# Kernel optimization log

Hardware: AMD Instinct MI355X
Metric: run time of the kernel (lower is better)

The kernel has to match this reference:

```python
import jax, jax.numpy as jnp
import numpy as np

B, L, D, Z, V, N, MAXPOS = 8, 2048, 1024, 128, 2048, 16, 2048


def setup_inputs():
    key = jax.random.key(0)
    ks = jax.random.split(key, 16)
    std = 0.02
    return {
        "x": jax.random.normal(ks[0], (B, L, D), jnp.float32),
        "norm1_w": jnp.ones((D,), jnp.float32),
        "norm1_b": jnp.zeros((D,), jnp.float32),
        "ema_delta": jax.random.normal(ks[1], (D, N), jnp.float32) * 0.2,
        "ema_alpha": jax.random.normal(ks[2], (D, N), jnp.float32) * 0.2,
        "ema_beta": jax.random.normal(ks[3], (D, N), jnp.float32) * 0.02,
        "ema_gamma": jax.random.normal(ks[4], (D, N), jnp.float32),
        "ema_omega": jax.random.normal(ks[5], (D,), jnp.float32),
        "vproj_w": jax.random.normal(ks[6], (D, V), jnp.float32) * std,
        "vproj_b": jnp.zeros((V,), jnp.float32),
        "mx_w": jax.random.normal(ks[7], (D, Z + V + 2 * D), jnp.float32) * std,
        "mx_b": jnp.zeros((Z + V + 2 * D,), jnp.float32),
        "h_w": jax.random.normal(ks[8], (V, D), jnp.float32) * std,
        "h_b": jnp.zeros((D,), jnp.float32),
        "att_gamma": jax.random.normal(ks[9], (2, Z), jnp.float32) * std,
        "att_beta": jnp.zeros((2, Z), jnp.float32),
        "rel_bias": jax.random.normal(ks[10], (2 * MAXPOS - 1,), jnp.float32) * std,
        "norm2_w": jnp.ones((D,), jnp.float32),
        "norm2_b": jnp.zeros((D,), jnp.float32),
        "ff_w1": jax.random.normal(ks[11], (D, 2 * D), jnp.float32) * std,
        "ff_b1": jnp.zeros((2 * D,), jnp.float32),
        "ff_w2": jax.random.normal(ks[12], (2 * D, D), jnp.float32) * std,
        "ff_b2": jnp.zeros((D,), jnp.float32),
    }


def _layernorm(x, w, b):
    mu = jnp.mean(x, -1, keepdims=True)
    var = jnp.mean((x - mu) ** 2, -1, keepdims=True)
    return (x - mu) * jax.lax.rsqrt(var + 1e-5) * w + b


def reference(x, norm1_w, norm1_b, ema_delta, ema_alpha, ema_beta, ema_gamma, ema_omega,
              vproj_w, vproj_b, mx_w, mx_b, h_w, h_b, att_gamma, att_beta, rel_bias,
              norm2_w, norm2_b, ff_w1, ff_b1, ff_w2, ff_b2):
    residual = x
    xn = _layernorm(x, norm1_w, norm1_b)                       # prenorm
    v = jax.nn.silu(xn @ vproj_w + vproj_b)                    # (B L V)

    # --- MultiHeadEMA (damped EMA state space) via FFT convolution ---
    p = jax.nn.sigmoid(ema_delta)                              # (D N)
    q = 1.0 - p * jax.nn.sigmoid(ema_alpha)                    # (D N) in (0,1)
    t = jnp.arange(L, dtype=jnp.float32)
    vander = jnp.exp(t[None, None, :] * jnp.log(q)[:, :, None])       # (D N L)
    kern = jnp.einsum('dnl,dn->dl', (p * ema_beta)[:, :, None] * vander,
                      ema_gamma * np.float32(1.0 / np.sqrt(N)))        # (D L)
    xT = jnp.swapaxes(xn, 1, 2)                                # (B D L)
    k_f = jnp.fft.rfft(kern, n=2 * L)
    x_f = jnp.fft.rfft(xT, n=2 * L)
    ema = jnp.fft.irfft(x_f * k_f, n=2 * L)[..., :L]           # causal conv
    mx = jax.nn.silu(jnp.swapaxes(ema, 1, 2) + xn * ema_omega) # (B L D)

    # --- moving-average gated attention ---
    base = mx @ mx_w + mx_b                                    # (B L D+Z+V+D)
    u, zr, hx = jnp.split(base, [D, D + Z + V], axis=-1)
    u = jax.nn.sigmoid(u)                                      # update gate
    zr = jax.nn.silu(zr)
    z, r = zr[..., :Z], zr[..., Z:]                            # (B L Z), (B L V)
    zqk = z[:, :, None, :] * att_gamma + att_beta              # (B L 2 Z)
    qh, kh = zqk[:, :, 0, :], zqk[:, :, 1, :]

    # simple relative positional bias: Toeplitz bias[i,j] = b[L-1 + j - i]
    bseg = rel_bias[MAXPOS - L:MAXPOS + L - 1]                 # (2L-1,)
    idx = (L - 1) + jnp.arange(L)[None, :] - jnp.arange(L)[:, None]
    bias = bseg[idx]                                           # (L L)

    qk = jnp.einsum('blz,bmz->blm', qh * np.float32(Z ** -0.5), kh) + bias
    attn = jax.nn.softmax(qk, axis=-1)                         # (B L L)
    h = jnp.einsum('blm,bmv->blv', attn, v)                    # (B L V)
    h = jax.nn.silu(hx + (h * r) @ h_w + h_b)                  # (B L D)
    out = residual + u * (h - residual)                        # addcmul gate

    # --- prenorm FFN residual block (expand=2, silu) ---
    y = _layernorm(out, norm2_w, norm2_b)
    y = jax.nn.silu(y @ ff_w1 + ff_b1) @ ff_w2 + ff_b2
    return out + y
```

## Files before the change

### kernel.cpp

```cpp
#include <hip/hip_runtime.h>
#include <hip/hip_bf16.h>
#include <cstdint>

#define B_ 8
#define L_ 2048
#define D_ 1024
#define Z_ 128
#define V_ 2048
#define N_ 16
#define NC_ 16
#define CL_ 128

typedef unsigned short ushort_t;
typedef __attribute__((ext_vector_type(8))) short short8;
typedef __attribute__((ext_vector_type(4))) float floatx4;

__device__ __forceinline__ float b2f(ushort_t u){ union{float f;unsigned i;}x; x.i=((unsigned)u)<<16; return x.f; }
__device__ __forceinline__ ushort_t f2b(float f){ union{float f;unsigned i;}x; x.f=f; unsigned r=(x.i+0x7fffu+((x.i>>16)&1u))>>16; return (ushort_t)r; }
__device__ __forceinline__ float sigmoidf_(float x){ return 1.0f/(1.0f+__expf(-x)); }
__device__ __forceinline__ float siluf_(float x){ return x/(1.0f+__expf(-x)); }

#define GLL16(g,l) __builtin_amdgcn_global_load_lds( \
    (const __attribute__((address_space(1))) void*)(g), \
    (__attribute__((address_space(3))) void*)(l), 16, 0, 0)

__device__ __forceinline__ float blockSum(float v){
  #pragma unroll
  for(int off=32;off;off>>=1) v += __shfl_xor(v,off);
  __shared__ float sm[4];
  __syncthreads();
  if((threadIdx.x&63)==0) sm[threadIdx.x>>6]=v;
  __syncthreads();
  return (sm[0]+sm[1])+(sm[2]+sm[3]);
}
__device__ __forceinline__ float blockMax(float v){
  #pragma unroll
  for(int off=32;off;off>>=1) v = fmaxf(v,__shfl_xor(v,off));
  __shared__ float sm[4];
  __syncthreads();
  if((threadIdx.x&63)==0) sm[threadIdx.x>>6]=v;
  __syncthreads();
  return fmaxf(fmaxf(sm[0],sm[1]),fmaxf(sm[2],sm[3]));
}

__global__ __launch_bounds__(256) void ln_kernel(const float* __restrict__ in,
    const float* __restrict__ w, const float* __restrict__ b,
    ushort_t* __restrict__ o16){
  const int row = blockIdx.x;
  const int t = threadIdx.x;
  const float* p = in + (size_t)row*D_;
  float4 v = *reinterpret_cast<const float4*>(p + t*4);
  float s = (v.x+v.y)+(v.z+v.w);
  s = blockSum(s);
  float mu = s*(1.0f/D_);
  float dx=v.x-mu, dy=v.y-mu, dz=v.z-mu, dw=v.w-mu;
  float ss = dx*dx+dy*dy+dz*dz+dw*dw;
  ss = blockSum(ss);
  float inv = rsqrtf(ss*(1.0f/D_)+1e-5f);
  float4 wv = *reinterpret_cast<const float4*>(w + t*4);
  float4 bv = *reinterpret_cast<const float4*>(b + t*4);
  union{ushort_t u[4]; uint2 q;} o;
  o.u[0]=f2b(dx*inv*wv.x+bv.x); o.u[1]=f2b(dy*inv*wv.y+bv.y);
  o.u[2]=f2b(dz*inv*wv.z+bv.z); o.u[3]=f2b(dw*inv*wv.w+bv.w);
  *reinterpret_cast<uint2*>(o16+(size_t)row*D_+t*4)=o.q;
}

__global__ __launch_bounds__(256) void transpose_w(const float* __restrict__ in,
    ushort_t* __restrict__ out, int R, int C){
  __shared__ float tile[32][33];
  int bx=blockIdx.x*32, by=blockIdx.y*32;
  int tx=threadIdx.x&31, ty=threadIdx.x>>5;
  #pragma unroll
  for(int i=0;i<32;i+=8) tile[ty+i][tx] = in[(size_t)(by+ty+i)*C + bx+tx];
  __syncthreads();
  #pragma unroll
  for(int i=0;i<32;i+=8) out[(size_t)(bx+ty+i)*R + by+tx] = f2b(tile[tx][ty+i]);
}

__global__ __launch_bounds__(256) void ema_setup(const float* __restrict__ delta,
    const float* __restrict__ alpha, const float* __restrict__ beta,
    const float* __restrict__ gamma, float* __restrict__ qarr,
    float* __restrict__ warr, float* __restrict__ qC){
  int i = blockIdx.x*256+threadIdx.x;
  if(i>=D_*N_) return;
  float p = sigmoidf_(delta[i]);
  float q = 1.0f - p*sigmoidf_(alpha[i]);
  qarr[i]=q; warr[i]=p*beta[i]*gamma[i]*0.25f;
  qC[i]=powf(q,(float)CL_);
}

__global__ __launch_bounds__(256) void ema_pass1(const ushort_t* __restrict__ xn,
    const float* __restrict__ qarr, float* __restrict__ E){
  int idx = blockIdx.x*256+threadIdx.x;
  int d = idx & (D_-1); int c = (idx>>10)&15; int b = idx>>14;
  const ushort_t* xp = xn + ((size_t)b*L_ + c*CL_)*D_ + d;
  float q[N_], s[N_];
  #pragma unroll
  for(int n=0;n<N_;n++){ q[n]=qarr[d*N_+n]; s[n]=0.0f; }
  for(int i=0;i<CL_;i+=8){
    float xv[8];
    #pragma unroll
    for(int j=0;j<8;j++) xv[j]=b2f(xp[(size_t)(i+j)*D_]);
    #pragma unroll
    for(int j=0;j<8;j++){
      #pragma unroll
      for(int n=0;n<N_;n++) s[n]=fmaf(q[n],s[n],xv[j]);
    }
  }
  float* Ep = E + (((size_t)b*NC_+c)*N_)*D_ + d;
  #pragma unroll
  for(int n=0;n<N_;n++) Ep[(size_t)n*D_]=s[n];
}

__global__ __launch_bounds__(256) void ema_pass2(const float* __restrict__ E,
    const float* __restrict__ qC, float* __restrict__ In){
  int idx = blockIdx.x*256+threadIdx.x;
  int d = idx & (D_-1); int b = idx>>10;
  float S[N_], qc[N_];
  #pragma unroll
  for(int n=0;n<N_;n++){ S[n]=0.0f; qc[n]=qC[d*N_+n]; }
  for(int c=0;c<NC_;c++){
    size_t base = (((size_t)b*NC_+c)*N_)*D_ + d;
    #pragma unroll
    for(int n=0;n<N_;n++) In[base+(size_t)n*D_]=S[n];
    #pragma unroll
    for(int n=0;n<N_;n++) S[n]=fmaf(qc[n],S[n],E[base+(size_t)n*D_]);
  }
}

__global__ __launch_bounds__(256) void ema_pass3_mx(const ushort_t* __restrict__ xn,
    const float* __restrict__ qarr, const float* __restrict__ warr,
    const float* __restrict__ In, const float* __restrict__ omega,
    ushort_t* __restrict__ mx){
  int idx = blockIdx.x*256+threadIdx.x;
  int d = idx & (D_-1); int c = (idx>>10)&15; int b = idx>>14;
  const ushort_t* xp = xn + ((size_t)b*L_ + c*CL_)*D_ + d;
  ushort_t* op = mx + ((size_t)b*L_ + c*CL_)*D_ + d;
  size_t base = (((size_t)b*NC_+c)*N_)*D_ + d;
  float om = omega[d];
  float q[N_], w[N_], s[N_];
  #pragma unroll
  for(int n=0;n<N_;n++){ q[n]=qarr[d*N_+n]; w[n]=warr[d*N_+n]; s[n]=In[base+(size_t)n*D_]; }
  for(int i=0;i<CL_;i+=8){
    float xv[8];
    #pragma unroll
    for(int j=0;j<8;j++) xv[j]=b2f(xp[(size_t)(i+j)*D_]);
    #pragma unroll
    for(int j=0;j<8;j++){
      float a=0.0f;
      #pragma unroll
      for(int n=0;n<N_;n++){ s[n]=fmaf(q[n],s[n],xv[j]); a=fmaf(w[n],s[n],a); }
      op[(size_t)(i+j)*D_]=f2b(siluf_(a + xv[j]*om));
    }
  }
}

__global__ __launch_bounds__(256) void softmax_kernel(const float* __restrict__ qk,
    ushort_t* __restrict__ attn){
  size_t row = blockIdx.x;
  const float* p = qk + row*(size_t)L_;
  int t = threadIdx.x;
  float vals[8];
  #pragma unroll
  for(int i=0;i<8;i++) vals[i]=p[i*256+t];
  float m=-__builtin_inff();
  #pragma unroll
  for(int i=0;i<8;i++) m=fmaxf(m,vals[i]);
  m = blockMax(m);
  float s=0.0f;
  #pragma unroll
  for(int i=0;i<8;i++){ vals[i]=__expf(vals[i]-m); s+=vals[i]; }
  s = blockSum(s);
  float inv = 1.0f/s;
  ushort_t* q = attn + row*(size_t)L_;
  #pragma unroll
  for(int i=0;i<8;i++) q[i*256+t]=f2b(vals[i]*inv);
}

#define SBAR() do{ __builtin_amdgcn_sched_barrier(0); \
    asm volatile("" ::: "memory"); \
    __builtin_amdgcn_s_barrier(); \
    asm volatile("" ::: "memory"); \
    __builtin_amdgcn_sched_barrier(0); }while(0)
#define VMW(n) asm volatile("s_waitcnt vmcnt(" #n ")" ::: "memory")

#define BAR_ACQ(vm) do{ \
    asm volatile("s_waitcnt vmcnt(" #vm ")" ::: "memory"); \
    __builtin_amdgcn_s_barrier(); \
    __builtin_amdgcn_sched_barrier(0); }while(0)
#define BAR_REL() do{ \
    __builtin_amdgcn_sched_barrier(0); \
    asm volatile("" ::: "memory"); \
    __builtin_amdgcn_s_barrier(); \
    asm volatile("" ::: "memory"); }while(0)

template<class Epi>
__global__ __launch_bounds__(256) void gemm_nt(const ushort_t* __restrict__ A,
    const ushort_t* __restrict__ B, int M, int N, int K, Epi epi){
  __shared__ __align__(16) ushort_t As[2][128*64];
  __shared__ __align__(16) ushort_t Bs[2][128*64];
  const int t = threadIdx.x;
  const int wave=t>>6, lane=t&63, quad=lane>>4, l16=lane&15;
  const int bm=blockIdx.x*128, bn=blockIdx.y*128;
  const int wm=(wave>>1)*64, wn=(wave&1)*64;
  const int srow = wave*32 + (lane>>3);
  const int schk = ((lane&7) ^ (lane>>3)) * 8;
  const ushort_t* gA[4]; const ushort_t* gB[4];
  ushort_t *lA[4], *lB[4];
  #pragma unroll
  for(int i=0;i<4;i++){
    gA[i] = A + (size_t)(bm+srow+i*8)*K + schk;
    gB[i] = B + (size_t)(bn+srow+i*8)*K + schk;
    lA[i] = &As[0][(wave*32+i*8)*64];
    lB[i] = &Bs[0][(wave*32+i*8)*64];
  }
  const ushort_t* ra[2][4]; const ushort_t* rb[2][4];
  #pragma unroll
  for(int h=0;h<2;h++)
    #pragma unroll
    for(int i=0;i<4;i++){
      int rrA = wm+i*16+l16, rrB = wn+i*16+l16;
      ra[h][i] = &As[0][rrA*64 + (((h*4+quad)^(rrA&7))*8)];
      rb[h][i] = &Bs[0][rrB*64 + (((h*4+quad)^(rrB&7))*8)];
    }
  floatx4 acc[4][4];
  #pragma unroll
  for(int i=0;i<4;i++)
    #pragma unroll
    for(int j=0;j<4;j++) acc[i][j]=(floatx4){0.f,0.f,0.f,0.f};

  const int nk = K>>6;
  #pragma unroll
  for(int i=0;i<4;i++){ GLL16(gA[i], lA[i]); GLL16(gB[i], lB[i]); }

  for(int t0=0;t0<nk;t0+=2){
    {
      const int k0=(t0+1)<<6;
      #pragma unroll
      for(int i=0;i<4;i++){ GLL16(gA[i]+k0, lA[i]+(128*64)); GLL16(gB[i]+k0, lB[i]+(128*64)); }
    }
    BAR_ACQ(8);
    #pragma unroll
    for(int h=0;h<2;h++){
      short8 af[4], bf[4];
      #pragma unroll
      for(int mt=0;mt<4;mt++) af[mt]=*reinterpret_cast<const short8*>(ra[h][mt]);
      #pragma unroll
      for(int nt=0;nt<4;nt++) bf[nt]=*reinterpret_cast<const short8*>(rb[h][nt]);
      #pragma unroll
      for(int mt=0;mt<4;mt++)
        #pragma unroll
        for(int nt=0;nt<4;nt++)
          acc[mt][nt]=__builtin_amdgcn_mfma_f32_16x16x32_bf16(af[mt],bf[nt],acc[mt][nt],0,0,0);
    }
    BAR_REL();
    if(t0+2<nk){
      const int k0=(t0+2)<<6;
      #pragma unroll
      for(int i=0;i<4;i++){ GLL16(gA[i]+k0, lA[i]); GLL16(gB[i]+k0, lB[i]); }
      BAR_ACQ(8);
    } else {
      BAR_ACQ(0);
    }
    #pragma unroll
    for(int h=0;h<2;h++){
      short8 af[4], bf[4];
      #pragma unroll
      for(int mt=0;mt<4;mt++) af[mt]=*reinterpret_cast<const short8*>(ra[h][mt]+(128*64));
      #pragma unroll
      for(int nt=0;nt<4;nt++) bf[nt]=*reinterpret_cast<const short8*>(rb[h][nt]+(128*64));
      #pragma unroll
      for(int mt=0;mt<4;mt++)
        #pragma unroll
        for(int nt=0;nt<4;nt++)
          acc[mt][nt]=__builtin_amdgcn_mfma_f32_16x16x32_bf16(af[mt],bf[nt],acc[mt][nt],0,0,0);
    }
    BAR_REL();
  }

  #pragma unroll
  for(int mt=0;mt<4;mt++)
    #pragma unroll
    for(int nt=0;nt<4;nt++)
      #pragma unroll
      for(int r=0;r<4;r++){
        int row=bm+wm+mt*16+quad*4+r;
        int col=bn+wn+nt*16+l16;
        epi(acc[mt][nt][r], row, col, 0);
      }
}


#define RDA4(buf,kh,mh) \
  af[0]=pA[(buf)*2048+(kh)*1024+((mh)*4+0)*64]; \
  af[1]=pA[(buf)*2048+(kh)*1024+((mh)*4+1)*64]; \
  af[2]=pA[(buf)*2048+(kh)*1024+((mh)*4+2)*64]; \
  af[3]=pA[(buf)*2048+(kh)*1024+((mh)*4+3)*64];
#define RDB4(buf,kh) \
  bf[0]=pB[(buf)*2048+(kh)*1024+0*64]; \
  bf[1]=pB[(buf)*2048+(kh)*1024+1*64]; \
  bf[2]=pB[(buf)*2048+(kh)*1024+2*64]; \
  bf[3]=pB[(buf)*2048+(kh)*1024+3*64];
#define MMA16(mh) \
  __builtin_amdgcn_s_setprio(1); \
  acc[(mh)*4+0][0]=__builtin_amdgcn_mfma_f32_16x16x32_bf16(af[0],bf[0],acc[(mh)*4+0][0],0,0,0); \
  acc[(mh)*4+0][1]=__builtin_amdgcn_mfma_f32_16x16x32_bf16(af[0],bf[1],acc[(mh)*4+0][1],0,0,0); \
  acc[(mh)*4+0][2]=__builtin_amdgcn_mfma_f32_16x16x32_bf16(af[0],bf[2],acc[(mh)*4+0][2],0,0,0); \
  acc[(mh)*4+0][3]=__builtin_amdgcn_mfma_f32_16x16x32_bf16(af[0],bf[3],acc[(mh)*4+0][3],0,0,0); \
  acc[(mh)*4+1][0]=__builtin_amdgcn_mfma_f32_16x16x32_bf16(af[1],bf[0],acc[(mh)*4+1][0],0,0,0); \
  acc[(mh)*4+1][1]=__builtin_amdgcn_mfma_f32_16x16x32_bf16(af[1],bf[1],acc[(mh)*4+1][1],0,0,0); \
  acc[(mh)*4+1][2]=__builtin_amdgcn_mfma_f32_16x16x32_bf16(af[1],bf[2],acc[(mh)*4+1][2],0,0,0); \
  acc[(mh)*4+1][3]=__builtin_amdgcn_mfma_f32_16x16x32_bf16(af[1],bf[3],acc[(mh)*4+1][3],0,0,0); \
  acc[(mh)*4+2][0]=__builtin_amdgcn_mfma_f32_16x16x32_bf16(af[2],bf[0],acc[(mh)*4+2][0],0,0,0); \
  acc[(mh)*4+2][1]=__builtin_amdgcn_mfma_f32_16x16x32_bf16(af[2],bf[1],acc[(mh)*4+2][1],0,0,0); \
  acc[(mh)*4+2][2]=__builtin_amdgcn_mfma_f32_16x16x32_bf16(af[2],bf[2],acc[(mh)*4+2][2],0,0,0); \
  acc[(mh)*4+2][3]=__builtin_amdgcn_mfma_f32_16x16x32_bf16(af[2],bf[3],acc[(mh)*4+2][3],0,0,0); \
  acc[(mh)*4+3][0]=__builtin_amdgcn_mfma_f32_16x16x32_bf16(af[3],bf[0],acc[(mh)*4+3][0],0,0,0); \
  acc[(mh)*4+3][1]=__builtin_amdgcn_mfma_f32_16x16x32_bf16(af[3],bf[1],acc[(mh)*4+3][1],0,0,0); \
  acc[(mh)*4+3][2]=__builtin_amdgcn_mfma_f32_16x16x32_bf16(af[3],bf[2],acc[(mh)*4+3][2],0,0,0); \
  acc[(mh)*4+3][3]=__builtin_amdgcn_mfma_f32_16x16x32_bf16(af[3],bf[3],acc[(mh)*4+3][3],0,0,0); \
  __builtin_amdgcn_s_setprio(0);
#define STG_A(rho,buf,kh,k0) GLL16(gA[rho] + (k0) + (kh)*32, lA[rho] + (buf)*16384 + (kh)*8192)
#define STG_B(rho,buf,kh,k0) GLL16(gB[rho] + (k0) + (kh)*32, lB[rho] + (buf)*16384 + (kh)*8192)
#define STG8(buf,k0) \
  STG_A(0,buf,0,k0); STG_A(1,buf,0,k0); STG_B(0,buf,0,k0); STG_B(1,buf,0,k0); \
  STG_A(0,buf,1,k0); STG_A(1,buf,1,k0); STG_B(0,buf,1,k0); STG_B(1,buf,1,k0);

#define TILE_S(buf,k0n) { \
  short8 af[4], bf[4]; \
  RDA4(buf,0,0) RDB4(buf,0) \
  STG8((buf)^1, k0n) \
  MMA16(0) \
  RDA4(buf,0,1) \
  MMA16(1) \
  VMW(8); SBAR(); \
  RDA4(buf,1,0) RDB4(buf,1) \
  MMA16(0) \
  RDA4(buf,1,1) \
  MMA16(1) \
  VMW(4); SBAR(); \
}
#define TILE_L(buf) { \
  short8 af[4], bf[4]; \
  RDA4(buf,0,0) RDB4(buf,0) \
  MMA16(0) \
  RDA4(buf,0,1) \
  MMA16(1) \
  VMW(0); SBAR(); \
  RDA4(buf,1,0) RDB4(buf,1) \
  MMA16(0) \
  RDA4(buf,1,1) \
  MMA16(1) \
}

template<class Epi>
__global__ __launch_bounds__(512) void gemm_nt2(const ushort_t* __restrict__ A0,
    const ushort_t* __restrict__ B0, int M, int N, int K,
    size_t za, size_t zb, Epi epi){
  __shared__ __align__(16) ushort_t As[2*2*8192];
  __shared__ __align__(16) ushort_t Bs[2*2*8192];
  const int t = threadIdx.x;
  const int wave=t>>6, lane=t&63, quad=lane>>4, l16=lane&15;
  const int z = blockIdx.z;
  const ushort_t* A = A0 + (size_t)z*za;
  const ushort_t* B = B0 + (size_t)z*zb;
  const int bm=blockIdx.x*256, bn=blockIdx.y*256;
  const int wm=(wave>>2)*128, wn=(wave&3)*64;
  const int srowl = wave*16 + (lane>>2);
  const int g8 = (((lane&3) ^ ((lane>>2)&3) ^ ((lane>>4)&1)))*8;
  const ushort_t* gA[2]; const ushort_t* gB[2];
  ushort_t* lA[2]; ushort_t* lB[2];
  #pragma unroll
  for(int rho=0;rho<2;rho++){
    gA[rho] = A + (size_t)(bm + rho*128 + srowl)*K + g8;
    gB[rho] = B + (size_t)(bn + rho*128 + srowl)*K + g8;
    lA[rho] = As + (rho*128 + wave*16)*32;
    lB[rho] = Bs + (rho*128 + wave*16)*32;
  }
  const int swl = (l16&3) ^ ((l16>>2)&1);
  const short8* pA = reinterpret_cast<const short8*>(As + (size_t)(wm+l16)*32 + (quad^swl)*8);
  const short8* pB = reinterpret_cast<const short8*>(Bs + (size_t)(wn+l16)*32 + (quad^swl)*8);
  floatx4 acc[8][4];
  #pragma unroll
  for(int i=0;i<8;i++)
    #pragma unroll
    for(int j=0;j<4;j++) acc[i][j]=(floatx4){0.f,0.f,0.f,0.f};

  const int nkt = K>>6;
  STG8(0, 0)
  VMW(4); SBAR();

  for(int t0=0; t0+2<nkt; t0+=2){
    TILE_S(0,(t0+1)<<6)
    TILE_S(1,(t0+2)<<6)
  }
  TILE_S(0,(nkt-1)<<6)
  TILE_L(1)

  #pragma unroll
  for(int mt=0;mt<8;mt++)
    #pragma unroll
    for(int nt=0;nt<4;nt++)
      #pragma unroll
      for(int r=0;r<4;r++){
        int row=bm+wm+mt*16+quad*4+r;
        int col=bn+wn+nt*16+l16;
        epi(acc[mt][nt][r], row, col, z);
      }
}

struct EpiV {
  ushort_t* vT; const float* vb;
  __device__ void operator()(float v,int row,int col,int) const {
    float s = siluf_(v + vb[col]);
    int b = row>>11, l = row&(L_-1);
    vT[((size_t)b*V_ + col)*L_ + l] = f2b(s);
  }
};
struct EpiU {
  ushort_t* u; const float* mxb;
  __device__ void operator()(float v,int row,int col,int) const {
    u[(size_t)row*D_+col]=f2b(sigmoidf_(v+mxb[col]));
  }
};
struct EpiQKh {
  ushort_t* qh; ushort_t* kh; const float* mxb; const float* ag; const float* ab;
  __device__ void operator()(float v,int row,int col,int) const {
    float z=siluf_(v+mxb[col]);
    qh[(size_t)row*Z_+col]=f2b(z*ag[col]+ab[col]);
    kh[(size_t)row*Z_+col]=f2b(z*ag[Z_+col]+ab[Z_+col]);
  }
};
struct EpiR {
  ushort_t* r; const float* mxb;
  __device__ void operator()(float v,int row,int col,int) const {
    r[(size_t)row*V_+col]=f2b(siluf_(v+mxb[col]));
  }
};
struct EpiHx {
  ushort_t* hx; const float* mxb;
  __device__ void operator()(float v,int row,int col,int) const {
    hx[(size_t)row*D_+col]=f2b(v+mxb[col]);
  }
};
struct EpiQK {
  float* qk; const float* rb;
  __device__ void operator()(float v,int row,int col,int) const {
    qk[(size_t)row*L_+col] = v*0.08838834764831845f + rb[L_-1+col-row];
  }
};
struct EpiH {
  ushort_t* hr; const ushort_t* r;
  __device__ void operator()(float v,int row,int col,int z) const {
    size_t idx = ((size_t)z*L_ + row)*V_ + col;
    hr[idx] = f2b(v * b2f(r[idx]));
  }
};
struct EpiOut {
  float* out; const float* x; const ushort_t* u; const ushort_t* hx; const float* hb;
  __device__ void operator()(float v,int row,int col,int) const {
    size_t idx=(size_t)row*D_+col;
    float h2 = siluf_(b2f(hx[idx]) + v + hb[col]);
    float xv = x[idx];
    out[idx] = xv + b2f(u[idx])*(h2-xv);
  }
};
struct EpiF1 {
  ushort_t* f1; const float* b1;
  __device__ void operator()(float v,int row,int col,int) const {
    f1[(size_t)row*(2*D_)+col]=f2b(siluf_(v+b1[col]));
  }
};
struct EpiFinal {
  float* dout; const float* b2;
  __device__ void operator()(float v,int row,int col,int) const {
    size_t idx=(size_t)row*D_+col;
    dout[idx] = dout[idx] + v + b2[col];
  }
};

extern "C" void kernel_launch(void* const* d_in, const int* in_sizes, int n_in,
                              void* d_out, int out_size, void* d_ws, size_t ws_size,
                              hipStream_t stream){
  const float* x        = (const float*)d_in[0];
  const float* norm1_w  = (const float*)d_in[1];
  const float* norm1_b  = (const float*)d_in[2];
  const float* ema_delta= (const float*)d_in[3];
  const float* ema_alpha= (const float*)d_in[4];
  const float* ema_beta = (const float*)d_in[5];
  const float* ema_gamma= (const float*)d_in[6];
  const float* ema_omega= (const float*)d_in[7];
  const float* vproj_w  = (const float*)d_in[8];
  const float* vproj_b  = (const float*)d_in[9];
  const float* mx_w     = (const float*)d_in[10];
  const float* mx_b     = (const float*)d_in[11];
  const float* h_w      = (const float*)d_in[12];
  const float* h_b      = (const float*)d_in[13];
  const float* att_gamma= (const float*)d_in[14];
  const float* att_beta = (const float*)d_in[15];
  const float* rel_bias = (const float*)d_in[16];
  const float* norm2_w  = (const float*)d_in[17];
  const float* norm2_b  = (const float*)d_in[18];
  const float* ff_w1    = (const float*)d_in[19];
  const float* ff_b1    = (const float*)d_in[20];
  const float* ff_w2    = (const float*)d_in[21];
  const float* ff_b2    = (const float*)d_in[22];
  float* dout = (float*)d_out;
  char* ws = (char*)d_ws;

  size_t cur = 0;
  auto take = [&](size_t b)->size_t{ size_t o=cur; cur += (b+255)&~255ull; return o; };
  const size_t o_wvT  = take((size_t)V_*D_*2);
  const size_t o_wmxT = take((size_t)4224*D_*2);
  const size_t o_whT  = take((size_t)D_*V_*2);
  const size_t o_wf1T = take((size_t)2*D_*D_*2);
  const size_t o_wf2T = take((size_t)D_*2*D_*2);
  const size_t o_qarr = take((size_t)D_*N_*4);
  const size_t o_warr = take((size_t)D_*N_*4);
  const size_t o_qC   = take((size_t)D_*N_*4);
  const size_t globals_end = cur;

  int g = 0;
  size_t o_xn=0,o_mx=0,o_u=0,o_hx=0,o_r=0,o_qh=0,o_kh=0,o_qk=0,o_at=0;
  for(int cand=8; cand>=1; cand>>=1){
    cur = globals_end;
    size_t xn_o = take((size_t)cand*L_*D_*2);
    size_t mx_o = take((size_t)cand*L_*D_*2);
    size_t u_o  = take((size_t)cand*L_*D_*2);
    size_t hx_o = take((size_t)cand*L_*D_*2);
    size_t r_o  = take((size_t)cand*L_*V_*2);
    size_t qh_o = take((size_t)cand*L_*Z_*2);
    size_t kh_o = take((size_t)cand*L_*Z_*2);
    size_t qk_o, at_o;
    if(cand>=4){ qk_o = xn_o; at_o = xn_o + (size_t)L_*L_*4; }
    else { qk_o = take((size_t)L_*L_*4); at_o = take((size_t)L_*L_*2); }
    if(cur <= ws_size){
      g=cand; o_xn=xn_o; o_mx=mx_o; o_u=u_o; o_hx=hx_o; o_r=r_o;
      o_qh=qh_o; o_kh=kh_o; o_qk=qk_o; o_at=at_o; break;
    }
  }
  if(!g) return;

  ushort_t* wvT  = (ushort_t*)(ws+o_wvT);
  ushort_t* wmxT = (ushort_t*)(ws+o_wmxT);
  ushort_t* whT  = (ushort_t*)(ws+o_whT);
  ushort_t* wf1T = (ushort_t*)(ws+o_wf1T);
  ushort_t* wf2T = (ushort_t*)(ws+o_wf2T);
  float* qarr = (float*)(ws+o_qarr);
  float* warr = (float*)(ws+o_warr);
  float* qC   = (float*)(ws+o_qC);
  ushort_t* xn  = (ushort_t*)(ws+o_xn);
  ushort_t* mx  = (ushort_t*)(ws+o_mx);
  ushort_t* u16 = (ushort_t*)(ws+o_u);
  ushort_t* hx16= (ushort_t*)(ws+o_hx);
  ushort_t* r16 = (ushort_t*)(ws+o_r);
  ushort_t* qh  = (ushort_t*)(ws+o_qh);
  ushort_t* kh  = (ushort_t*)(ws+o_kh);
  float*    qk  = (float*)   (ws+o_qk);
  ushort_t* attn= (ushort_t*)(ws+o_at);
  float*    E   = (float*)(ws+o_u);
  float*    In  = (float*)(ws+o_hx);
  ushort_t* ybf = xn;
  ushort_t* f1  = r16;

  int nbat; ushort_t* attnB;
  if(g>=4){ nbat = g/2; attnB = mx; }
  else    { nbat = 1;   attnB = attn; }

  transpose_w<<<dim3(V_/32, D_/32), 256, 0, stream>>>(vproj_w, wvT, D_, V_);
  transpose_w<<<dim3(4224/32, D_/32), 256, 0, stream>>>(mx_w, wmxT, D_, 4224);
  transpose_w<<<dim3(D_/32, V_/32), 256, 0, stream>>>(h_w, whT, V_, D_);
  transpose_w<<<dim3((2*D_)/32, D_/32), 256, 0, stream>>>(ff_w1, wf1T, D_, 2*D_);
  transpose_w<<<dim3(D_/32, (2*D_)/32), 256, 0, stream>>>(ff_w2, wf2T, 2*D_, D_);
  ema_setup<<<(D_*N_)/256, 256, 0, stream>>>(ema_delta, ema_alpha, ema_beta, ema_gamma, qarr, warr, qC);

  for(int gi=0; gi<B_/g; ++gi){
    const int RG = g*L_;
    const float* x_g  = x    + (size_t)gi*RG*D_;
    float*       do_g = dout + (size_t)gi*RG*D_;
    ushort_t*    vT   = (ushort_t*)do_g;

    ln_kernel<<<RG, 256, 0, stream>>>(x_g, norm1_w, norm1_b, xn);
    ema_pass1<<<(g*NC_*D_)/256, 256, 0, stream>>>(xn, qarr, E);
    ema_pass2<<<(g*D_)/256, 256, 0, stream>>>(E, qC, In);
    ema_pass3_mx<<<(g*NC_*D_)/256, 256, 0, stream>>>(xn, qarr, warr, In, ema_omega, mx);

    { EpiV e{vT, vproj_b};
      gemm_nt2<<<dim3(RG/256, V_/256), 512, 0, stream>>>(xn, wvT, RG, V_, D_, 0, 0, e); }

    { EpiU e{u16, mx_b};
      gemm_nt2<<<dim3(RG/256, D_/256), 512, 0, stream>>>(mx, wmxT, RG, D_, D_, 0, 0, e); }
    { EpiQKh e{qh, kh, mx_b+D_, att_gamma, att_beta};
      gemm_nt<<<dim3(RG/128, Z_/128), 256, 0, stream>>>(mx, wmxT+(size_t)D_*D_, RG, Z_, D_, e); }
    { EpiR e{r16, mx_b+D_+Z_};
      gemm_nt2<<<dim3(RG/256, V_/256), 512, 0, stream>>>(mx, wmxT+(size_t)(D_+Z_)*D_, RG, V_, D_, 0, 0, e); }
    { EpiHx e{hx16, mx_b+D_+Z_+V_};
      gemm_nt2<<<dim3(RG/256, D_/256), 512, 0, stream>>>(mx, wmxT+(size_t)(D_+Z_+V_)*D_, RG, D_, D_, 0, 0, e); }

    for(int q0=0; q0<g; q0+=nbat){
      for(int bi=q0; bi<q0+nbat; ++bi){
        { EpiQK e{qk, rel_bias};
          gemm_nt<<<dim3(L_/128, L_/128), 256, 0, stream>>>(
            qh+(size_t)bi*L_*Z_, kh+(size_t)bi*L_*Z_, L_, L_, Z_, e); }
        softmax_kernel<<<L_, 256, 0, stream>>>(qk, attnB+(size_t)(bi-q0)*L_*L_);
      }
      { EpiH e{r16+(size_t)q0*L_*V_, r16+(size_t)q0*L_*V_};
        gemm_nt2<<<dim3(L_/256, V_/256, nbat), 512, 0, stream>>>(
          attnB, vT+(size_t)q0*V_*L_, L_, V_, L_,
          (size_t)L_*L_, (size_t)V_*L_, e); }
    }

    { EpiOut e{do_g, x_g, u16, hx16, h_b};
      gemm_nt2<<<dim3(RG/256, D_/256), 512, 0, stream>>>(r16, whT, RG, D_, V_, 0, 0, e); }
    ln_kernel<<<RG, 256, 0, stream>>>(do_g, norm2_w, norm2_b, ybf);
    { EpiF1 e{f1, ff_b1};
      gemm_nt2<<<dim3(RG/256, (2*D_)/256), 512, 0, stream>>>(ybf, wf1T, RG, 2*D_, D_, 0, 0, e); }
    { EpiFinal e{do_g, ff_b2};
      gemm_nt2<<<dim3(RG/256, D_/256), 512, 0, stream>>>(f1, wf2T, RG, D_, 2*D_, 0, 0, e); }
  }
}
```

Measured before the change: 1.350 ms.

## Restructure main GEMM LDS layout, add grouped tile swizzle, and barrier-interleave MFMA phases

```diff
diff --git a/kernel.cpp b/kernel.cpp
--- a/kernel.cpp
+++ b/kernel.cpp
@@ -291,16 +291,16 @@
 }
 
 
-#define RDA4(buf,kh,mh) \
-  af[0]=pA[(buf)*2048+(kh)*1024+((mh)*4+0)*64]; \
-  af[1]=pA[(buf)*2048+(kh)*1024+((mh)*4+1)*64]; \
-  af[2]=pA[(buf)*2048+(kh)*1024+((mh)*4+2)*64]; \
-  af[3]=pA[(buf)*2048+(kh)*1024+((mh)*4+3)*64];
-#define RDB4(buf,kh) \
-  bf[0]=pB[(buf)*2048+(kh)*1024+0*64]; \
-  bf[1]=pB[(buf)*2048+(kh)*1024+1*64]; \
-  bf[2]=pB[(buf)*2048+(kh)*1024+2*64]; \
-  bf[3]=pB[(buf)*2048+(kh)*1024+3*64];
+#define RDA(buf,kh,mh) \
+  af[0]=pA##kh[(buf)*2048+((mh)*4+0)*128]; \
+  af[1]=pA##kh[(buf)*2048+((mh)*4+1)*128]; \
+  af[2]=pA##kh[(buf)*2048+((mh)*4+2)*128]; \
+  af[3]=pA##kh[(buf)*2048+((mh)*4+3)*128];
+#define RDB(buf,kh) \
+  bf[0]=pB##kh[(buf)*2048+0*128]; \
+  bf[1]=pB##kh[(buf)*2048+1*128]; \
+  bf[2]=pB##kh[(buf)*2048+2*128]; \
+  bf[3]=pB##kh[(buf)*2048+3*128];
 #define MMA16(mh) \
   __builtin_amdgcn_s_setprio(1); \
   acc[(mh)*4+0][0]=__builtin_amdgcn_mfma_f32_16x16x32_bf16(af[0],bf[0],acc[(mh)*4+0][0],0,0,0); \
@@ -320,66 +320,76 @@
   acc[(mh)*4+3][2]=__builtin_amdgcn_mfma_f32_16x16x32_bf16(af[3],bf[2],acc[(mh)*4+3][2],0,0,0); \
   acc[(mh)*4+3][3]=__builtin_amdgcn_mfma_f32_16x16x32_bf16(af[3],bf[3],acc[(mh)*4+3][3],0,0,0); \
   __builtin_amdgcn_s_setprio(0);
-#define STG_A(rho,buf,kh,k0) GLL16(gA[rho] + (k0) + (kh)*32, lA[rho] + (buf)*16384 + (kh)*8192)
-#define STG_B(rho,buf,kh,k0) GLL16(gB[rho] + (k0) + (kh)*32, lB[rho] + (buf)*16384 + (kh)*8192)
 #define STG8(buf,k0) \
-  STG_A(0,buf,0,k0); STG_A(1,buf,0,k0); STG_B(0,buf,0,k0); STG_B(1,buf,0,k0); \
-  STG_A(0,buf,1,k0); STG_A(1,buf,1,k0); STG_B(0,buf,1,k0); STG_B(1,buf,1,k0);
+  GLL16(gA[0]+(k0), lA[0]+(buf)*16384); GLL16(gA[1]+(k0), lA[1]+(buf)*16384); \
+  GLL16(gA[2]+(k0), lA[2]+(buf)*16384); GLL16(gA[3]+(k0), lA[3]+(buf)*16384); \
+  GLL16(gB[0]+(k0), lB[0]+(buf)*16384); GLL16(gB[1]+(k0), lB[1]+(buf)*16384); \
+  GLL16(gB[2]+(k0), lB[2]+(buf)*16384); GLL16(gB[3]+(k0), lB[3]+(buf)*16384);
 
 #define TILE_S(buf,k0n) { \
   short8 af[4], bf[4]; \
-  RDA4(buf,0,0) RDB4(buf,0) \
+  RDA(buf,0,0) RDB(buf,0) \
   STG8((buf)^1, k0n) \
-  MMA16(0) \
-  RDA4(buf,0,1) \
-  MMA16(1) \
-  VMW(8); SBAR(); \
-  RDA4(buf,1,0) RDB4(buf,1) \
-  MMA16(0) \
-  RDA4(buf,1,1) \
-  MMA16(1) \
-  VMW(4); SBAR(); \
+  SBAR(); MMA16(0) SBAR(); \
+  RDA(buf,0,1) \
+  SBAR(); MMA16(1) SBAR(); \
+  RDA(buf,1,0) RDB(buf,1) \
+  SBAR(); MMA16(0) SBAR(); \
+  RDA(buf,1,1) \
+  SBAR(); MMA16(1) VMW(0); SBAR(); \
 }
 #define TILE_L(buf) { \
   short8 af[4], bf[4]; \
-  RDA4(buf,0,0) RDB4(buf,0) \
-  MMA16(0) \
-  RDA4(buf,0,1) \
-  MMA16(1) \
-  VMW(0); SBAR(); \
-  RDA4(buf,1,0) RDB4(buf,1) \
-  MMA16(0) \
-  RDA4(buf,1,1) \
-  MMA16(1) \
+  RDA(buf,0,0) RDB(buf,0) \
+  SBAR(); MMA16(0) SBAR(); \
+  RDA(buf,0,1) \
+  SBAR(); MMA16(1) SBAR(); \
+  RDA(buf,1,0) RDB(buf,1) \
+  SBAR(); MMA16(0) SBAR(); \
+  RDA(buf,1,1) \
+  SBAR(); MMA16(1) \
 }
 
 template<class Epi>
 __global__ __launch_bounds__(512) void gemm_nt2(const ushort_t* __restrict__ A0,
     const ushort_t* __restrict__ B0, int M, int N, int K,
     size_t za, size_t zb, Epi epi){
-  __shared__ __align__(16) ushort_t As[2*2*8192];
-  __shared__ __align__(16) ushort_t Bs[2*2*8192];
+  __shared__ __align__(16) ushort_t As[2*256*64];
+  __shared__ __align__(16) ushort_t Bs[2*256*64];
   const int t = threadIdx.x;
   const int wave=t>>6, lane=t&63, quad=lane>>4, l16=lane&15;
+  int bx, by;
+  {
+    int gx=gridDim.x, gy=gridDim.y;
+    int f = blockIdx.y*gx + blockIdx.x;
+    if((gy==4 || gy==8) && (gx%(32/gy))==0){
+      int GW = 32/gy, nst = gx/GW;
+      int s, r;
+      if((nst&7)==0){ int xc=f&7; int j=f>>3; s = xc*(nst>>3) + (j>>5); r = j&31; }
+      else { s = f>>5; r = f&31; }
+      bx = s*GW + (r%GW); by = r/GW;
+    } else { bx = blockIdx.x; by = blockIdx.y; }
+  }
   const int z = blockIdx.z;
   const ushort_t* A = A0 + (size_t)z*za;
   const ushort_t* B = B0 + (size_t)z*zb;
-  const int bm=blockIdx.x*256, bn=blockIdx.y*256;
+  const int bm=bx*256, bn=by*256;
   const int wm=(wave>>2)*128, wn=(wave&3)*64;
-  const int srowl = wave*16 + (lane>>2);
-  const int g8 = (((lane&3) ^ ((lane>>2)&3) ^ ((lane>>4)&1)))*8;
-  const ushort_t* gA[2]; const ushort_t* gB[2];
-  ushort_t* lA[2]; ushort_t* lB[2];
-  #pragma unroll
-  for(int rho=0;rho<2;rho++){
-    gA[rho] = A + (size_t)(bm + rho*128 + srowl)*K + g8;
-    gB[rho] = B + (size_t)(bn + rho*128 + srowl)*K + g8;
-    lA[rho] = As + (rho*128 + wave*16)*32;
-    lB[rho] = Bs + (rho*128 + wave*16)*32;
-  }
-  const int swl = (l16&3) ^ ((l16>>2)&1);
-  const short8* pA = reinterpret_cast<const short8*>(As + (size_t)(wm+l16)*32 + (quad^swl)*8);
-  const short8* pB = reinterpret_cast<const short8*>(Bs + (size_t)(wn+l16)*32 + (quad^swl)*8);
+  const int roff = lane>>3;
+  const int goff = ((lane&7)^(lane>>3))*8;
+  const ushort_t* gA[4]; const ushort_t* gB[4];
+  ushort_t* lA[4]; ushort_t* lB[4];
+  #pragma unroll
+  for(int i=0;i<4;i++){
+    gA[i] = A + (size_t)(bm + wave*32 + i*8 + roff)*K + goff;
+    gB[i] = B + (size_t)(bn + wave*32 + i*8 + roff)*K + goff;
+    lA[i] = As + (wave*32 + i*8)*64;
+    lB[i] = Bs + (wave*32 + i*8)*64;
+  }
+  const short8* pA0 = reinterpret_cast<const short8*>(As) + (wm+l16)*8 + ((quad  )^(l16&7));
+  const short8* pA1 = reinterpret_cast<const short8*>(As) + (wm+l16)*8 + ((quad^4)^(l16&7));
+  const short8* pB0 = reinterpret_cast<const short8*>(Bs) + (wn+l16)*8 + ((quad  )^(l16&7));
+  const short8* pB1 = reinterpret_cast<const short8*>(Bs) + (wn+l16)*8 + ((quad^4)^(l16&7));
   floatx4 acc[8][4];
   #pragma unroll
   for(int i=0;i<8;i++)
@@ -388,7 +398,7 @@
 
   const int nkt = K>>6;
   STG8(0, 0)
-  VMW(4); SBAR();
+  VMW(0); SBAR();
 
   for(int t0=0; t0+2<nkt; t0+=2){
     TILE_S(0,(t0+1)<<6)
```

Result: no change. 1.354 ms (+0.3%).
